# Optimization experiments

Hardware: AMD Instinct MI355X
Metric: run time of the kernel (lower is better)

Reference implementation:

```python
import jax, jax.numpy as jnp
import numpy as np

N, M, D = 8192, 8192, 64


def setup_inputs() -> dict:
    key = jax.random.key(0)
    kx, ky = jax.random.split(key)
    X = jax.random.normal(kx, (N, D), dtype=jnp.float32)
    Y = jax.random.normal(ky, (M, D), dtype=jnp.float32)
    return {"X": X, "Y": Y}


def reference(X, Y):
    # Pairwise Euclidean distances via the |x|^2 + |y|^2 - 2<x,y> identity
    # (avoids materializing the [N, M, D] difference tensor).
    x2 = jnp.sum(X * X, axis=1)[:, None]          # [N, 1]
    y2 = jnp.sum(Y * Y, axis=1)[None, :]          # [1, M]
    d2 = x2 + y2 - 2.0 * (X @ Y.T)                # [N, M]
    d = jnp.sqrt(jnp.maximum(d2, 0.0))            # Euclidean distance matrix
    dis_1 = jnp.mean(jnp.min(d, axis=1))          # avg over X of nearest-in-Y
    dis_2 = jnp.mean(jnp.min(d, axis=0))          # avg over Y of nearest-in-X
    return dis_1 + dis_2
```

## Files before the change

### kernel.cpp

```cpp
#include <hip/hip_runtime.h>
#include <math.h>


#define NROWS 8192
#define DDIM  64
#define ITILES 64
#define SLICES 16
#define CHUNKS 4
#define LSTR 72

typedef __bf16 bf16_t;
typedef bf16_t bf16x8 __attribute__((ext_vector_type(8)));
typedef float  f32x4  __attribute__((ext_vector_type(4)));

__global__ void prep_kernel(const float* __restrict__ X,
                            const float* __restrict__ Y,
                            bf16_t* __restrict__ Xbf, bf16_t* __restrict__ Ybf,
                            float* __restrict__ x2, float* __restrict__ y2,
                            float* __restrict__ out) {
  int t = blockIdx.x * blockDim.x + threadIdx.x;
  int half = t >> 15;
  int r = (t >> 2) & (NROWS - 1);
  int part = t & 3;
  const float* src = half ? Y : X;
  bf16_t* dst = half ? Ybf : Xbf;
  float* sq = half ? y2 : x2;

  const float4* p = (const float4*)(src + r * DDIM + part * 16);
  float4 v0 = p[0], v1 = p[1], v2 = p[2], v3 = p[3];
  float s = 0.f;
  s = fmaf(v0.x, v0.x, s); s = fmaf(v0.y, v0.y, s);
  s = fmaf(v0.z, v0.z, s); s = fmaf(v0.w, v0.w, s);
  s = fmaf(v1.x, v1.x, s); s = fmaf(v1.y, v1.y, s);
  s = fmaf(v1.z, v1.z, s); s = fmaf(v1.w, v1.w, s);
  s = fmaf(v2.x, v2.x, s); s = fmaf(v2.y, v2.y, s);
  s = fmaf(v2.z, v2.z, s); s = fmaf(v2.w, v2.w, s);
  s = fmaf(v3.x, v3.x, s); s = fmaf(v3.y, v3.y, s);
  s = fmaf(v3.z, v3.z, s); s = fmaf(v3.w, v3.w, s);

  bf16x8 h0 = {(bf16_t)v0.x, (bf16_t)v0.y, (bf16_t)v0.z, (bf16_t)v0.w,
               (bf16_t)v1.x, (bf16_t)v1.y, (bf16_t)v1.z, (bf16_t)v1.w};
  bf16x8 h1 = {(bf16_t)v2.x, (bf16_t)v2.y, (bf16_t)v2.z, (bf16_t)v2.w,
               (bf16_t)v3.x, (bf16_t)v3.y, (bf16_t)v3.z, (bf16_t)v3.w};
  *(bf16x8*)&dst[r * DDIM + part * 16] = h0;
  *(bf16x8*)&dst[r * DDIM + part * 16 + 8] = h1;

  s += __shfl_xor(s, 1, 64);
  s += __shfl_xor(s, 2, 64);
  if (part == 0) sq[r] = s;
  if (t == 0) out[0] = 0.f;
}

__global__ __launch_bounds__(256, 2)
void mine_kernel(const bf16_t* __restrict__ Xbf, const bf16_t* __restrict__ Ybf,
                 const float* __restrict__ x2g, const float* __restrict__ y2g,
                 float* __restrict__ rslab, float* __restrict__ cslab) {
  __shared__ bf16_t Ys[2][128 * LSTR];

  const int tid = threadIdx.x;
  const int L = tid & 63;
  const int w = tid >> 6;
  const int lr = L & 15;
  const int q = L >> 4;
  const int rh = w >> 1;
  const int ch = w & 1;
  const int itile = blockIdx.x & (ITILES - 1);
  const int slice = blockIdx.x >> 6;
  const int i0 = itile * 128;
  const int rgb = rh * 64;
  const int cgb = ch * 64;
  const int jbase = slice * (CHUNKS * 128);

  bf16x8 Af[8];
#pragma unroll
  for (int a = 0; a < 4; ++a) {
    int row = i0 + rgb + a * 16 + lr;
#pragma unroll
    for (int h = 0; h < 2; ++h)
      Af[a * 2 + h] = *(const bf16x8*)&Xbf[row * DDIM + h * 32 + q * 8];
  }
  float x2r[16];
#pragma unroll
  for (int a = 0; a < 4; ++a) {
    float4 v = *(const float4*)&x2g[i0 + rgb + a * 16 + q * 4];
    x2r[a * 4 + 0] = v.x; x2r[a * 4 + 1] = v.y;
    x2r[a * 4 + 2] = v.z; x2r[a * 4 + 3] = v.w;
  }
  float y2all[CHUNKS][4];
#pragma unroll
  for (int cc = 0; cc < CHUNKS; ++cc)
#pragma unroll
    for (int b = 0; b < 4; ++b)
      y2all[cc][b] = y2g[jbase + cc * 128 + cgb + b * 16 + lr];

  float rmin[16];
#pragma unroll
  for (int k = 0; k < 16; ++k) rmin[k] = INFINITY;

  bf16x8 Bst[4];
#pragma unroll
  for (int p = 0; p < 4; ++p) {
    int f = p * 256 + tid;
    Bst[p] = *(const bf16x8*)&Ybf[(jbase + (f >> 3)) * DDIM + (f & 7) * 8];
  }
#pragma unroll
  for (int p = 0; p < 4; ++p) {
    int f = p * 256 + tid;
    *(bf16x8*)&Ys[0][(f >> 3) * LSTR + (f & 7) * 8] = Bst[p];
  }
  __syncthreads();

  for (int cc = 0; cc < CHUNKS; ++cc) {
    const bf16_t* Yb = Ys[cc & 1];
    if (cc + 1 < CHUNKS) {
      int j0n = jbase + (cc + 1) * 128;
#pragma unroll
      for (int p = 0; p < 4; ++p) {
        int f = p * 256 + tid;
        Bst[p] = *(const bf16x8*)&Ybf[(j0n + (f >> 3)) * DDIM + (f & 7) * 8];
      }
    }

    f32x4 acc[4][4];
#pragma unroll
    for (int a = 0; a < 4; ++a)
#pragma unroll
      for (int b = 0; b < 4; ++b) acc[a][b] = (f32x4){0.f, 0.f, 0.f, 0.f};

#pragma unroll
    for (int b = 0; b < 4; ++b) {
      bf16x8 B0 = *(const bf16x8*)&Yb[(cgb + b * 16 + lr) * LSTR + q * 8];
      bf16x8 B1 = *(const bf16x8*)&Yb[(cgb + b * 16 + lr) * LSTR + 32 + q * 8];
#pragma unroll
      for (int a = 0; a < 4; ++a) {
        acc[a][b] = __builtin_amdgcn_mfma_f32_16x16x32_bf16(Af[a * 2 + 0], B0, acc[a][b], 0, 0, 0);
        acc[a][b] = __builtin_amdgcn_mfma_f32_16x16x32_bf16(Af[a * 2 + 1], B1, acc[a][b], 0, 0, 0);
      }
    }

    float cmin[4] = {INFINITY, INFINITY, INFINITY, INFINITY};
#pragma unroll
    for (int a = 0; a < 4; ++a)
#pragma unroll
      for (int p = 0; p < 4; ++p) {
        float x2v = x2r[a * 4 + p];
        float rm = rmin[a * 4 + p];
#pragma unroll
        for (int b = 0; b < 4; ++b) {
          float s = acc[a][b][p];
          rm = fminf(rm, fmaf(-2.f, s, y2all[cc][b]));
          cmin[b] = fminf(cmin[b], fmaf(-2.f, s, x2v));
        }
        rmin[a * 4 + p] = rm;
      }
#pragma unroll
    for (int b = 0; b < 4; ++b) {
      cmin[b] = fminf(cmin[b], __shfl_xor(cmin[b], 16, 64));
      cmin[b] = fminf(cmin[b], __shfl_xor(cmin[b], 32, 64));
    }
    float v = cmin[0];
    if (q == 1) v = cmin[1];
    else if (q == 2) v = cmin[2];
    else if (q == 3) v = cmin[3];
    cslab[(itile * 2 + rh) * NROWS + jbase + cc * 128 + cgb + L] = v;

    if (cc + 1 < CHUNKS) {
      bf16_t* Yn = Ys[(cc + 1) & 1];
#pragma unroll
      for (int p = 0; p < 4; ++p) {
        int f = p * 256 + tid;
        *(bf16x8*)&Yn[(f >> 3) * LSTR + (f & 7) * 8] = Bst[p];
      }
      __syncthreads();
    }
  }

#pragma unroll
  for (int a = 0; a < 4; ++a)
#pragma unroll
    for (int p = 0; p < 4; ++p) {
      float v = rmin[a * 4 + p];
      v = fminf(v, __shfl_xor(v, 1, 64));
      v = fminf(v, __shfl_xor(v, 2, 64));
      v = fminf(v, __shfl_xor(v, 4, 64));
      v = fminf(v, __shfl_xor(v, 8, 64));
      if (lr == 0)
        rslab[slice * (NROWS * 2) + (i0 + rgb + a * 16 + q * 4 + p) * 2 + ch] = v;
    }
}

__global__ void finish_kernel(const float* __restrict__ x2,
                              const float* __restrict__ y2,
                              const float* __restrict__ rslab,
                              const float* __restrict__ cslab,
                              float* __restrict__ out) {
  const int b = blockIdx.x;
  const int tid = threadIdx.x;
  if (b < 32) {
    int row = b * 256 + tid;
    float m = INFINITY;
#pragma unroll
    for (int g = 0; g < SLICES; ++g) {
      float2 v = *(const float2*)&rslab[g * (NROWS * 2) + row * 2];
      m = fminf(m, fminf(v.x, v.y));
    }
    float v = sqrtf(fmaxf(x2[row] + m, 0.f)) * (1.0f / 8192.0f);
#pragma unroll
    for (int off = 32; off > 0; off >>= 1) v += __shfl_down(v, off, 64);
    __shared__ float partial[4];
    if ((tid & 63) == 0) partial[tid >> 6] = v;
    __syncthreads();
    if (tid == 0)
      atomicAdd(out, partial[0] + partial[1] + partial[2] + partial[3]);
  } else {
    int j = (b - 32) * 64 + (tid & 63);
    int seg = tid >> 6;
    float m = INFINITY;
#pragma unroll
    for (int k = 0; k < 32; ++k)
      m = fminf(m, cslab[(seg * 32 + k) * NROWS + j]);
    __shared__ float red[4][64];
    red[seg][tid & 63] = m;
    __syncthreads();
    if (tid < 64) {
      float mc = fminf(fminf(red[0][tid], red[1][tid]),
                       fminf(red[2][tid], red[3][tid]));
      float v = sqrtf(fmaxf(y2[j] + mc, 0.f)) * (1.0f / 8192.0f);
#pragma unroll
      for (int off = 32; off > 0; off >>= 1) v += __shfl_down(v, off, 64);
      if (tid == 0) atomicAdd(out, v);
    }
  }
}

extern "C" void kernel_launch(void* const* d_in, const int* in_sizes, int n_in,
                              void* d_out, int out_size, void* d_ws, size_t ws_size,
                              hipStream_t stream) {
  const float* X = (const float*)d_in[0];
  const float* Y = (const float*)d_in[1];
  float* out = (float*)d_out;

  char* wsb = (char*)d_ws;
  bf16_t* Xbf = (bf16_t*)wsb;
  bf16_t* Ybf = (bf16_t*)(wsb + (size_t)NROWS * DDIM * 2);
  float* x2 = (float*)(wsb + 2 * (size_t)NROWS * DDIM * 2);
  float* y2 = x2 + NROWS;
  float* rslab = y2 + NROWS;
  float* cslab = rslab + SLICES * NROWS * 2;

  prep_kernel<<<(2 * NROWS * 4) / 256, 256, 0, stream>>>(X, Y, Xbf, Ybf, x2, y2, out);
  mine_kernel<<<ITILES * SLICES, 256, 0, stream>>>(Xbf, Ybf, x2, y2, rslab, cslab);
  finish_kernel<<<160, 256, 0, stream>>>(x2, y2, rslab, cslab, out);
}
```

Baseline: 84.48 us.

## Halve slices, combine column minima in LDS before writing to global

The Y range is now split into 8 slices of 8 chunks each instead of 16 slices of 4, which halves the grid and the partial-result slabs. The two row-halves of each block now combine their per-column minima through shared memory before one global store, halving the cslab writes and the finish kernel's reads. y2 values are loaded per chunk instead of all up front, and the min reductions are reordered into shorter dependency chains. The cost is a barrier every chunk and fewer blocks, so less parallelism to hide latency.

```diff
diff --git a/kernel.cpp b/kernel.cpp
--- a/kernel.cpp
+++ b/kernel.cpp
@@ -5,8 +5,8 @@
 #define NROWS 8192
 #define DDIM  64
 #define ITILES 64
-#define SLICES 16
-#define CHUNKS 4
+#define SLICES 8
+#define CHUNKS 8
 #define LSTR 72
 
 typedef __bf16 bf16_t;
@@ -56,6 +56,7 @@
                  const float* __restrict__ x2g, const float* __restrict__ y2g,
                  float* __restrict__ rslab, float* __restrict__ cslab) {
   __shared__ bf16_t Ys[2][128 * LSTR];
+  __shared__ float credL[2][2][128];
 
   const int tid = threadIdx.x;
   const int L = tid & 63;
@@ -86,12 +87,6 @@
     x2r[a * 4 + 0] = v.x; x2r[a * 4 + 1] = v.y;
     x2r[a * 4 + 2] = v.z; x2r[a * 4 + 3] = v.w;
   }
-  float y2all[CHUNKS][4];
-#pragma unroll
-  for (int cc = 0; cc < CHUNKS; ++cc)
-#pragma unroll
-    for (int b = 0; b < 4; ++b)
-      y2all[cc][b] = y2g[jbase + cc * 128 + cgb + b * 16 + lr];
 
   float rmin[16];
 #pragma unroll
@@ -112,6 +107,12 @@
 
   for (int cc = 0; cc < CHUNKS; ++cc) {
     const bf16_t* Yb = Ys[cc & 1];
+
+    float y2c[4];
+#pragma unroll
+    for (int b = 0; b < 4; ++b)
+      y2c[b] = y2g[jbase + cc * 128 + cgb + b * 16 + lr];
+
     if (cc + 1 < CHUNKS) {
       int j0n = jbase + (cc + 1) * 128;
 #pragma unroll
@@ -140,19 +141,27 @@
 
     float cmin[4] = {INFINITY, INFINITY, INFINITY, INFINITY};
 #pragma unroll
-    for (int a = 0; a < 4; ++a)
+    for (int a = 0; a < 4; ++a) {
 #pragma unroll
       for (int p = 0; p < 4; ++p) {
-        float x2v = x2r[a * 4 + p];
+        float t0 = fmaf(-2.f, acc[a][0][p], y2c[0]);
+        float t1 = fmaf(-2.f, acc[a][1][p], y2c[1]);
+        float t2 = fmaf(-2.f, acc[a][2][p], y2c[2]);
+        float t3 = fmaf(-2.f, acc[a][3][p], y2c[3]);
         float rm = rmin[a * 4 + p];
-#pragma unroll
-        for (int b = 0; b < 4; ++b) {
-          float s = acc[a][b][p];
-          rm = fminf(rm, fmaf(-2.f, s, y2all[cc][b]));
-          cmin[b] = fminf(cmin[b], fmaf(-2.f, s, x2v));
-        }
-        rmin[a * 4 + p] = rm;
-      }
+        rm = fminf(fminf(rm, t0), t1);
+        rmin[a * 4 + p] = fminf(fminf(rm, t2), t3);
+      }
+#pragma unroll
+      for (int b = 0; b < 4; ++b) {
+        float u0 = fmaf(-2.f, acc[a][b][0], x2r[a * 4 + 0]);
+        float u1 = fmaf(-2.f, acc[a][b][1], x2r[a * 4 + 1]);
+        float u2 = fmaf(-2.f, acc[a][b][2], x2r[a * 4 + 2]);
+        float u3 = fmaf(-2.f, acc[a][b][3], x2r[a * 4 + 3]);
+        cmin[b] = fminf(fminf(cmin[b], u0), u1);
+        cmin[b] = fminf(fminf(cmin[b], u2), u3);
+      }
+    }
 #pragma unroll
     for (int b = 0; b < 4; ++b) {
       cmin[b] = fminf(cmin[b], __shfl_xor(cmin[b], 16, 64));
@@ -162,7 +171,7 @@
     if (q == 1) v = cmin[1];
     else if (q == 2) v = cmin[2];
     else if (q == 3) v = cmin[3];
-    cslab[(itile * 2 + rh) * NROWS + jbase + cc * 128 + cgb + L] = v;
+    credL[cc & 1][rh][cgb + L] = v;
 
     if (cc + 1 < CHUNKS) {
       bf16_t* Yn = Ys[(cc + 1) & 1];
@@ -171,7 +180,12 @@
         int f = p * 256 + tid;
         *(bf16x8*)&Yn[(f >> 3) * LSTR + (f & 7) * 8] = Bst[p];
       }
-      __syncthreads();
+    }
+    __syncthreads();
+
+    if (tid < 128) {
+      float m = fminf(credL[cc & 1][0][tid], credL[cc & 1][1][tid]);
+      cslab[itile * NROWS + jbase + cc * 128 + tid] = m;
     }
   }
 
@@ -217,8 +231,8 @@
     int seg = tid >> 6;
     float m = INFINITY;
 #pragma unroll
-    for (int k = 0; k < 32; ++k)
-      m = fminf(m, cslab[(seg * 32 + k) * NROWS + j]);
+    for (int k = 0; k < 16; ++k)
+      m = fminf(m, cslab[(seg * 16 + k) * NROWS + j]);
     __shared__ float red[4][64];
     red[seg][tid & 63] = m;
     __syncthreads();
```

New measurement: 80.33 us. 1.05x faster.
